# Optimization experiments

Measured on AMD Instinct MI355X. Metric: run time of the kernel, lower is better.

## Reference

```python
import jax, jax.numpy as jnp
import numpy as np

B, N, C, F, E, K = 2, 2048, 1024, 4096, 8, 2

def setup_inputs() -> dict:
    key = jax.random.key(0)
    k = jax.random.split(key, 6)
    xavier1 = float(np.sqrt(6.0 / (C + F)))
    xavier2 = float(np.sqrt(6.0 / (F + C)))
    return {
        "x": jax.random.normal(k[0], (B, N, C), dtype=jnp.float32),
        "router_w": jax.random.normal(k[1], (E, C), dtype=jnp.float32) * 0.01,
        "w1": jax.random.uniform(k[2], (E, F, C), dtype=jnp.float32, minval=-xavier1, maxval=xavier1),
        "b1": jnp.zeros((E, F), dtype=jnp.float32),
        "w2": jax.random.uniform(k[3], (E, C, F), dtype=jnp.float32, minval=-xavier2, maxval=xavier2),
        "b2": jnp.zeros((E, C), dtype=jnp.float32),
    }

def reference(x, router_w, w1, b1, w2, b2):
    Bb, Nn, Cc = x.shape
    x_flat = x.reshape(-1, Cc)                                   # [T, C]
    # Router (eval mode: no noise)
    logits = jnp.einsum('tc,ec->te', x_flat, router_w)           # [T, E]
    probs = jax.nn.softmax(logits, axis=-1)
    top_w, top_idx = jax.lax.top_k(probs, K)                     # [T, K]
    top_w = top_w / (jnp.sum(top_w, axis=-1, keepdims=True) + 1e-9)
    # Dense all-expert MLP (same math as the per-expert gather/scatter loop)
    h = jnp.einsum('tc,efc->tef', x_flat, w1) + b1[None]          # [T, E, F]
    h = jax.nn.relu(h)
    y = jnp.einsum('tef,ecf->tec', h, w2) + b2[None]              # [T, E, C]
    # Gather the K selected experts per token and combine
    sel = jnp.take_along_axis(y, top_idx[:, :, None], axis=1)    # [T, K, C]
    out = jnp.einsum('tkc,tk->tc', sel, top_w)                   # [T, C]
    return out.reshape(Bb, Nn, Cc)
```

## Files before the change

kernel.cpp:

```cpp
#include <hip/hip_runtime.h>
#include <hip/hip_fp16.h>


#define T_TOK 4096
#define C_DIM 1024
#define F_DIM 4096
#define E_NUM 8
#define BM 128
#define BN 256
#define BK 64
#define MAXT 72
#define NP   (MAXT * BM)
#define TILE_H 8192

typedef float f32x4 __attribute__((ext_vector_type(4)));
typedef _Float16 half8 __attribute__((ext_vector_type(8)));

#define AS1 __attribute__((address_space(1)))
#define AS3 __attribute__((address_space(3)))

__device__ __forceinline__ int swz(int r, int ec) { return ec ^ ((r & 7) << 3); }

__device__ __forceinline__ half8 cvt8(float4 f0, float4 f1) {
  half8 hv;
  hv[0] = (_Float16)f0.x; hv[1] = (_Float16)f0.y; hv[2] = (_Float16)f0.z; hv[3] = (_Float16)f0.w;
  hv[4] = (_Float16)f1.x; hv[5] = (_Float16)f1.y; hv[6] = (_Float16)f1.z; hv[7] = (_Float16)f1.w;
  return hv;
}

__device__ __forceinline__ int xcd_swz(int bid, int nwg) {
  int xcd = bid & 7, rest = bid >> 3;
  int q = nwg >> 3, r = nwg & 7;
  return (xcd < r ? xcd * (q + 1) : r * (q + 1) + (xcd - r) * q) + rest;
}

__global__ __launch_bounds__(256) void router_kernel(
    const float* __restrict__ x, const float* __restrict__ rw,
    int* __restrict__ top_idx, float* __restrict__ top_w)
{
  int t = blockIdx.x * 4 + (threadIdx.x >> 6);
  int lane = threadIdx.x & 63;
  const float* xr = x + (size_t)t * C_DIM;
  float acc[E_NUM];
#pragma unroll
  for (int e = 0; e < E_NUM; ++e) acc[e] = 0.f;
  for (int j = 0; j < C_DIM / 64; ++j) {
    int c = j * 64 + lane;
    float xv = xr[c];
#pragma unroll
    for (int e = 0; e < E_NUM; ++e) acc[e] += xv * rw[e * C_DIM + c];
  }
#pragma unroll
  for (int e = 0; e < E_NUM; ++e) {
    float v = acc[e];
#pragma unroll
    for (int off = 32; off > 0; off >>= 1) v += __shfl_xor(v, off);
    acc[e] = v;
  }
  if (lane == 0) {
    float mx = acc[0];
    for (int e = 1; e < E_NUM; ++e) mx = fmaxf(mx, acc[e]);
    float p[E_NUM]; float Z = 0.f;
    for (int e = 0; e < E_NUM; ++e) { p[e] = expf(acc[e] - mx); Z += p[e]; }
    int b0 = 0;
    for (int e = 1; e < E_NUM; ++e) if (p[e] > p[b0]) b0 = e;
    int b1i = -1; float pb = -1.f;
    for (int e = 0; e < E_NUM; ++e) if (e != b0 && p[e] > pb) { pb = p[e]; b1i = e; }
    float p0 = p[b0] / Z, p1 = pb / Z;
    float s = p0 + p1 + 1e-9f;
    top_idx[t * 2 + 0] = b0;
    top_idx[t * 2 + 1] = b1i;
    top_w[t * 2 + 0] = p0 / s;
    top_w[t * 2 + 1] = p1 / s;
  }
}

__global__ void build_lists(const int* __restrict__ top_idx,
                            int* __restrict__ rows_g, int* __restrict__ counts,
                            int* __restrict__ tile_off, int* __restrict__ inv)
{
  int e = threadIdx.x >> 6;
  int lane = threadIdx.x & 63;
  int cnt = 0;
  for (int t0 = 0; t0 < T_TOK; t0 += 64) {
    int t = t0 + lane;
    bool sel = (top_idx[t * 2] == e) || (top_idx[t * 2 + 1] == e);
    cnt += __popcll(__ballot(sel));
  }
  if (lane == 0) counts[e] = cnt;
  __syncthreads();
  if (threadIdx.x == 0) {
    int o = 0;
    for (int i = 0; i < E_NUM; ++i) { tile_off[i] = o; o += (counts[i] + BM - 1) / BM; }
    tile_off[E_NUM] = o;
  }
  __syncthreads();
  int base = tile_off[e] * BM;
  int pos = 0;
  for (int t0 = 0; t0 < T_TOK; t0 += 64) {
    int t = t0 + lane;
    int i0 = top_idx[t * 2], i1 = top_idx[t * 2 + 1];
    bool sel = (i0 == e) || (i1 == e);
    unsigned long long mask = __ballot(sel);
    if (sel) {
      int p = pos + __popcll(mask & ((1ull << lane) - 1ull));
      int slot = t * 2 + ((i0 == e) ? 0 : 1);
      rows_g[base + p] = slot;
      inv[slot] = (e << 16) | (base + p);
    }
    pos += __popcll(mask);
  }
}

__global__ __launch_bounds__(256) void gather_x(
    const float* __restrict__ x, const int* __restrict__ rows_g,
    const int* __restrict__ counts, const int* __restrict__ tile_off,
    _Float16* __restrict__ xg)
{
  unsigned g = blockIdx.x * 256 + threadIdx.x;
  unsigned p = g >> 7, ccr = g & 127;
  int gt = p >> 7, r = p & 127;
  int kc = ccr >> 3, c8 = ccr & 7;
  int e = -1;
#pragma unroll
  for (int i = 0; i < E_NUM; ++i)
    if (gt >= tile_off[i] && gt < tile_off[i + 1]) e = i;
  half8 hv = {};
  if (e >= 0) {
    int nrem = counts[e] - (gt - tile_off[e]) * BM;
    if (r < nrem) {
      int t = rows_g[p] >> 1;
      const float4* s = reinterpret_cast<const float4*>(x + (size_t)t * C_DIM + kc * 64 + c8 * 8);
      hv = cvt8(s[0], s[1]);
    }
  }
  *reinterpret_cast<half8*>(xg + ((size_t)gt * 16 + kc) * TILE_H + r * 64 + ((c8 ^ (r & 7)) << 3)) = hv;
}

__global__ __launch_bounds__(256) void cvt_w1(
    const float* __restrict__ src, _Float16* __restrict__ dst, int ch, int Fc, int lgnftl)
{
  unsigned g = blockIdx.x * 256 + threadIdx.x;
  unsigned tile = g >> 10;
  unsigned kc = tile & 15;
  unsigned et = tile >> 4;
  unsigned ftl = et & ((1u << lgnftl) - 1);
  unsigned e = et >> lgnftl;
  unsigned r = (g >> 3) & 127;
  unsigned sc = g & 7;
  unsigned c8 = sc ^ (r & 7);
  unsigned frow = ftl * 128 + r;
  const float4* s = reinterpret_cast<const float4*>(
      src + ((size_t)e * F_DIM + ch * Fc + frow) * C_DIM + kc * 64 + c8 * 8);
  *reinterpret_cast<half8*>(dst + (size_t)g * 8) = cvt8(s[0], s[1]);
}

__global__ __launch_bounds__(256) void cvt_w2(
    const float* __restrict__ src, _Float16* __restrict__ dst, int ch, int Fc, int lgnkc)
{
  unsigned g = blockIdx.x * 256 + threadIdx.x;
  unsigned tile = g >> 10;
  unsigned kc = tile & ((1u << lgnkc) - 1);
  unsigned et = tile >> lgnkc;
  unsigned ct = et & 7;
  unsigned e = et >> 3;
  unsigned r = (g >> 3) & 127;
  unsigned sc = g & 7;
  unsigned c8 = sc ^ (r & 7);
  unsigned c = ct * 128 + r;
  const float4* s = reinterpret_cast<const float4*>(
      src + ((size_t)e * C_DIM + c) * F_DIM + ch * Fc + kc * 64 + c8 * 8);
  *reinterpret_cast<half8*>(dst + (size_t)g * 8) = cvt8(s[0], s[1]);
}

#define STAGE_TILE(aSrc_, b0Src_, b1Src_)                                         \
  {                                                                               \
    _Pragma("unroll")                                                             \
    for (int i_ = 0; i_ < 2; ++i_) {                                              \
      int o_ = tid * 8 + i_ * 4096;                                               \
      __builtin_amdgcn_global_load_lds((const AS1 void*)((aSrc_) + o_),           \
          (AS3 void*)(&As[o_]), 16, 0, 0);                                        \
      __builtin_amdgcn_global_load_lds((const AS1 void*)((b0Src_) + o_),          \
          (AS3 void*)(&Bs[o_]), 16, 0, 0);                                        \
      __builtin_amdgcn_global_load_lds((const AS1 void*)((b1Src_) + o_),          \
          (AS3 void*)(&Bs[8192 + o_]), 16, 0, 0);                                 \
    }                                                                             \
  }

#define COMPUTE_TILE()                                                            \
  _Pragma("unroll")                                                               \
  for (int kk = 0; kk < BK; kk += 32) {                                           \
    const int klo = kk + (lane >> 4) * 8;                                         \
    half8 aF[4], bF[4];                                                           \
    _Pragma("unroll")                                                             \
    for (int m = 0; m < 4; ++m) {                                                 \
      int r = wr * 64 + m * 16 + (lane & 15);                                     \
      aF[m] = *reinterpret_cast<const half8*>(&As[r * BK + swz(r, klo)]);         \
    }                                                                             \
    _Pragma("unroll")                                                             \
    for (int n = 0; n < 4; ++n) {                                                 \
      int br = wc * 64 + n * 16 + (lane & 15);                                    \
      bF[n] = *reinterpret_cast<const half8*>(                                    \
          &Bs[(br >> 7) * 8192 + (br & 127) * 64 + swz(br, klo)]);                \
    }                                                                             \
    _Pragma("unroll")                                                             \
    for (int m = 0; m < 4; ++m)                                                   \
      _Pragma("unroll")                                                           \
      for (int n = 0; n < 4; ++n)                                                 \
        acc[m][n] = __builtin_amdgcn_mfma_f32_16x16x32_f16(aF[m], bF[n], acc[m][n], 0, 0, 0); \
  }

#define STAGE2(aSrc_, bSrc_)                                                      \
  {                                                                               \
    _Pragma("unroll")                                                             \
    for (int i_ = 0; i_ < 4; ++i_) {                                              \
      int o_ = tid * 8 + i_ * 2048;                                               \
      __builtin_amdgcn_global_load_lds((const AS1 void*)((aSrc_) + o_),           \
          (AS3 void*)(&As[o_]), 16, 0, 0);                                        \
      __builtin_amdgcn_global_load_lds((const AS1 void*)((bSrc_) + o_),           \
          (AS3 void*)(&Bs[o_]), 16, 0, 0);                                        \
    }                                                                             \
  }

#define COMPUTE2()                                                                \
  _Pragma("unroll")                                                               \
  for (int kk = 0; kk < BK; kk += 32) {                                           \
    const int klo = kk + (lane >> 4) * 8;                                         \
    half8 aF[4], bF[4];                                                           \
    _Pragma("unroll")                                                             \
    for (int m = 0; m < 4; ++m) {                                                 \
      int r = wr * 64 + m * 16 + (lane & 15);                                     \
      aF[m] = *reinterpret_cast<const half8*>(&As[r * BK + swz(r, klo)]);         \
    }                                                                             \
    _Pragma("unroll")                                                             \
    for (int n = 0; n < 4; ++n) {                                                 \
      int r = wc * 64 + n * 16 + (lane & 15);                                     \
      bF[n] = *reinterpret_cast<const half8*>(&Bs[r * BK + swz(r, klo)]);         \
    }                                                                             \
    _Pragma("unroll")                                                             \
    for (int m = 0; m < 4; ++m)                                                   \
      _Pragma("unroll")                                                           \
      for (int n = 0; n < 4; ++n)                                                 \
        acc[m][n] = __builtin_amdgcn_mfma_f32_16x16x32_f16(aF[m], bF[n], acc[m][n], 0, 0, 0); \
  }

__global__ __launch_bounds__(512) void gemm1_kernel(
    const _Float16* __restrict__ xg, const _Float16* __restrict__ w1t,
    const float* __restrict__ b1, const int* __restrict__ counts,
    const int* __restrict__ tile_off, _Float16* __restrict__ ht,
    int ch, int Fc)
{
  const int NFT = Fc / BN;
  const int wgid = xcd_swz(blockIdx.x, gridDim.x);
  const int grp = wgid / (8 * NFT);
  const int rem = wgid - grp * 8 * NFT;
  const int ft = rem >> 3;
  const int gt = grp * 8 + (rem & 7);
  if (gt >= tile_off[E_NUM]) return;
  int e = 0;
  while (gt >= tile_off[e + 1]) ++e;
  const int nrem = min(counts[e] - (gt - tile_off[e]) * BM, BM);
  const int nftl = Fc >> 7;
  const _Float16* At  = xg + (size_t)gt * 16 * TILE_H;
  const _Float16* Bt0 = w1t + (size_t)(e * nftl + 2 * ft) * 16 * TILE_H;
  const _Float16* Bt1 = w1t + (size_t)(e * nftl + 2 * ft + 1) * 16 * TILE_H;

  __shared__ __align__(16) _Float16 As[TILE_H];
  __shared__ __align__(16) _Float16 Bs[2 * TILE_H];

  const int tid = threadIdx.x;
  const int lane = tid & 63;
  const int wave = tid >> 6;
  const int wr = wave >> 2, wc = wave & 3;

  f32x4 acc[4][4];
#pragma unroll
  for (int m = 0; m < 4; ++m)
#pragma unroll
    for (int n = 0; n < 4; ++n) acc[m][n] = (f32x4){0.f, 0.f, 0.f, 0.f};

  for (int kc = 0; kc < 16; ++kc) {
    STAGE_TILE(At + (size_t)kc * TILE_H, Bt0 + (size_t)kc * TILE_H, Bt1 + (size_t)kc * TILE_H);
    __syncthreads();
    COMPUTE_TILE();
    __syncthreads();
  }

  const int nkcF = Fc >> 6;
#pragma unroll
  for (int m = 0; m < 4; ++m) {
#pragma unroll
    for (int j = 0; j < 4; ++j) {
      int iloc = wr * 64 + m * 16 + (lane >> 4) * 4 + j;
      if (iloc < nrem) {
#pragma unroll
        for (int n = 0; n < 4; ++n) {
          int fl = ft * BN + wc * 64 + n * 16 + (lane & 15);
          float v = acc[m][n][j] + b1[e * F_DIM + ch * Fc + fl];
          _Float16 h = (_Float16)fmaxf(v, 0.f);
          ht[((size_t)gt * nkcF + (fl >> 6)) * TILE_H + iloc * 64 +
             ((((fl >> 3) & 7) ^ (iloc & 7)) << 3) + (fl & 7)] = h;
        }
      }
    }
  }
}

__global__ __launch_bounds__(256) void gemm2_kernel(
    const _Float16* __restrict__ ht, const _Float16* __restrict__ w2t,
    const int* __restrict__ tile_off, _Float16* __restrict__ y,
    int Fc, int kspl, int accum)
{
  const int NCMB = 8 * kspl;
  const int wgid = xcd_swz(blockIdx.x, gridDim.x);
  const int grp = wgid / (8 * NCMB);
  const int rem = wgid - grp * 8 * NCMB;
  const int cmb = rem >> 3;
  const int gt = grp * 8 + (rem & 7);
  if (gt >= tile_off[E_NUM]) return;
  const int ct = cmb & 7;
  const int ks = cmb >> 3;
  int e = 0;
  while (gt >= tile_off[e + 1]) ++e;
  const int nkc = Fc >> 6;
  const int klen = nkc / kspl;
  const _Float16* At = ht + ((size_t)gt * nkc + ks * klen) * TILE_H;
  const _Float16* Bt = w2t + ((size_t)(e * 8 + ct) * nkc + ks * klen) * TILE_H;

  __shared__ __align__(16) _Float16 As[TILE_H];
  __shared__ __align__(16) _Float16 Bs[TILE_H];

  const int tid = threadIdx.x;
  const int lane = tid & 63;
  const int wave = tid >> 6;
  const int wr = wave >> 1, wc = wave & 1;

  f32x4 acc[4][4];
#pragma unroll
  for (int m = 0; m < 4; ++m)
#pragma unroll
    for (int n = 0; n < 4; ++n) acc[m][n] = (f32x4){0.f, 0.f, 0.f, 0.f};

  for (int kc = 0; kc < klen; ++kc) {
    STAGE2(At + (size_t)kc * TILE_H, Bt + (size_t)kc * TILE_H);
    __syncthreads();
    COMPUTE2();
    __syncthreads();
  }

  _Float16* yk = y + ((size_t)(ks * MAXT + gt) * BM) * C_DIM;
#pragma unroll
  for (int m = 0; m < 4; ++m) {
#pragma unroll
    for (int j = 0; j < 4; ++j) {
      int iloc = wr * 64 + m * 16 + (lane >> 4) * 4 + j;
#pragma unroll
      for (int n = 0; n < 4; ++n) {
        int c = ct * 128 + wc * 64 + n * 16 + (lane & 15);
        _Float16* p = yk + (size_t)iloc * C_DIM + c;
        float v = acc[m][n][j];
        if (accum) v += (float)*p;
        *p = (_Float16)v;
      }
    }
  }
}

__global__ __launch_bounds__(256) void combine_kernel(
    const _Float16* __restrict__ y, const int* __restrict__ inv,
    const float* __restrict__ top_w, const float* __restrict__ b2,
    float* __restrict__ out, int kspl)
{
  int g = blockIdx.x * 256 + threadIdx.x;
  int t = g >> 7, c8 = (g & 127) << 3;
  float o[8];
#pragma unroll
  for (int i = 0; i < 8; ++i) o[i] = 0.f;
#pragma unroll
  for (int k = 0; k < 2; ++k) {
    int iv = inv[t * 2 + k];
    int e = iv >> 16, pos = iv & 0xffff;
    float w = top_w[t * 2 + k];
    const float4* bb = reinterpret_cast<const float4*>(b2 + e * C_DIM + c8);
    float4 bv0 = bb[0], bv1 = bb[1];
    float s[8] = {bv0.x, bv0.y, bv0.z, bv0.w, bv1.x, bv1.y, bv1.z, bv1.w};
    for (int ks = 0; ks < kspl; ++ks) {
      half8 hv = *reinterpret_cast<const half8*>(
          y + ((size_t)(ks * MAXT * BM + pos)) * C_DIM + c8);
#pragma unroll
      for (int i = 0; i < 8; ++i) s[i] += (float)hv[i];
    }
#pragma unroll
    for (int i = 0; i < 8; ++i) o[i] += w * s[i];
  }
  float4* op = reinterpret_cast<float4*>(out + (size_t)t * C_DIM + c8);
  op[0] = (float4){o[0], o[1], o[2], o[3]};
  op[1] = (float4){o[4], o[5], o[6], o[7]};
}

extern "C" void kernel_launch(void* const* d_in, const int* in_sizes, int n_in,
                              void* d_out, int out_size, void* d_ws, size_t ws_size,
                              hipStream_t stream)
{
  const float* x  = (const float*)d_in[0];
  const float* rw = (const float*)d_in[1];
  const float* w1 = (const float*)d_in[2];
  const float* b1 = (const float*)d_in[3];
  const float* w2 = (const float*)d_in[4];
  const float* b2 = (const float*)d_in[5];
  float* out = (float*)d_out;

  char* ws = (char*)d_ws;
  size_t off = 0;
  auto carve = [&](size_t bytes) -> void* {
    void* p = ws + off;
    off += (bytes + 255) & ~(size_t)255;
    return p;
  };
  int*   top_idx  = (int*)carve((size_t)T_TOK * 2 * sizeof(int));
  float* top_w    = (float*)carve((size_t)T_TOK * 2 * sizeof(float));
  int*   counts   = (int*)carve(E_NUM * sizeof(int));
  int*   tile_off = (int*)carve((E_NUM + 1) * sizeof(int));
  int*   rows_g   = (int*)carve((size_t)NP * sizeof(int));
  int*   inv      = (int*)carve((size_t)T_TOK * 2 * sizeof(int));
  _Float16* xg    = (_Float16*)carve((size_t)MAXT * 16 * TILE_H * sizeof(_Float16));
  _Float16* y     = (_Float16*)carve((size_t)2 * NP * C_DIM * sizeof(_Float16));
  size_t fixed = off;

  int nchunk = 8;
  const int cands[4] = {1, 2, 4, 8};
  for (int ci = 0; ci < 4; ++ci) {
    int n = cands[ci];
    size_t fc = (size_t)(F_DIM / n);
    size_t w1b = ((size_t)E_NUM * fc * C_DIM * 2 + 255) & ~(size_t)255;
    size_t w2b = ((size_t)E_NUM * C_DIM * fc * 2 + 255) & ~(size_t)255;
    size_t htb = ((size_t)MAXT * (fc >> 6) * TILE_H * 2 + 255) & ~(size_t)255;
    if (fixed + w1b + w2b + htb <= ws_size) { nchunk = n; break; }
  }
  const int Fc = F_DIM / nchunk;
  int lgFc = 0; while ((1 << lgFc) < Fc) ++lgFc;
  _Float16* w1t = (_Float16*)carve((size_t)E_NUM * Fc * C_DIM * sizeof(_Float16));
  _Float16* w2t = (_Float16*)carve((size_t)E_NUM * C_DIM * Fc * sizeof(_Float16));
  _Float16* ht  = (_Float16*)carve((size_t)MAXT * (Fc >> 6) * TILE_H * sizeof(_Float16));

  const int kspl = (Fc >= 2048) ? 2 : 1;

  router_kernel<<<T_TOK / 4, 256, 0, stream>>>(x, rw, top_idx, top_w);
  build_lists<<<1, 512, 0, stream>>>(top_idx, rows_g, counts, tile_off, inv);
  gather_x<<<(MAXT * BM * 128) / 256, 256, 0, stream>>>(x, rows_g, counts, tile_off, xg);

  const int cvt_blocks = 4 * Fc;
  for (int ch = 0; ch < nchunk; ++ch) {
    cvt_w1<<<cvt_blocks, 256, 0, stream>>>(w1, w1t, ch, Fc, lgFc - 7);
    cvt_w2<<<cvt_blocks, 256, 0, stream>>>(w2, w2t, ch, Fc, lgFc - 6);
    gemm1_kernel<<<MAXT * (Fc / BN), 512, 0, stream>>>(
        xg, w1t, b1, counts, tile_off, ht, ch, Fc);
    gemm2_kernel<<<MAXT * 8 * kspl, 256, 0, stream>>>(
        ht, w2t, tile_off, y, Fc, kspl, ch != 0);
  }
  combine_kernel<<<(T_TOK * 128) / 256, 256, 0, stream>>>(y, inv, top_w, b2, out, kspl);
}
```

Baseline: 355.5 us.

## Swap MFMA operands for vectorized epilogue stores and merge weight conversion kernels

The MFMA operand order is swapped so each lane's four accumulator values lie along the feature/channel dimension. The gemm1 and gemm2 epilogues can then issue half4 stores, float4 bias loads and half4 read-modify-writes instead of scalar per-element accesses. The two weight-conversion kernels are merged into one launch per chunk to cut launch overhead. The gemm1 row-validity check is dropped, so padded rows now write relu(bias) into ht; these rows appear to be discarded downstream.

Result: no change. 352.7 us (-0.8%).

```diff
diff --git a/kernel.cpp b/kernel.cpp
--- a/kernel.cpp
+++ b/kernel.cpp
@@ -15,6 +15,7 @@
 
 typedef float f32x4 __attribute__((ext_vector_type(4)));
 typedef _Float16 half8 __attribute__((ext_vector_type(8)));
+typedef _Float16 half4 __attribute__((ext_vector_type(4)));
 
 #define AS1 __attribute__((address_space(1)))
 #define AS3 __attribute__((address_space(3)))
@@ -137,40 +138,40 @@
   *reinterpret_cast<half8*>(xg + ((size_t)gt * 16 + kc) * TILE_H + r * 64 + ((c8 ^ (r & 7)) << 3)) = hv;
 }
 
-__global__ __launch_bounds__(256) void cvt_w1(
-    const float* __restrict__ src, _Float16* __restrict__ dst, int ch, int Fc, int lgnftl)
+__global__ __launch_bounds__(256) void cvt_w(
+    const float* __restrict__ w1, const float* __restrict__ w2,
+    _Float16* __restrict__ w1t, _Float16* __restrict__ w2t,
+    int ch, int Fc, int lgnftl, int lgnkc, unsigned halfChunks)
 {
   unsigned g = blockIdx.x * 256 + threadIdx.x;
-  unsigned tile = g >> 10;
-  unsigned kc = tile & 15;
-  unsigned et = tile >> 4;
-  unsigned ftl = et & ((1u << lgnftl) - 1);
-  unsigned e = et >> lgnftl;
-  unsigned r = (g >> 3) & 127;
-  unsigned sc = g & 7;
-  unsigned c8 = sc ^ (r & 7);
-  unsigned frow = ftl * 128 + r;
-  const float4* s = reinterpret_cast<const float4*>(
-      src + ((size_t)e * F_DIM + ch * Fc + frow) * C_DIM + kc * 64 + c8 * 8);
-  *reinterpret_cast<half8*>(dst + (size_t)g * 8) = cvt8(s[0], s[1]);
-}
-
-__global__ __launch_bounds__(256) void cvt_w2(
-    const float* __restrict__ src, _Float16* __restrict__ dst, int ch, int Fc, int lgnkc)
-{
-  unsigned g = blockIdx.x * 256 + threadIdx.x;
-  unsigned tile = g >> 10;
-  unsigned kc = tile & ((1u << lgnkc) - 1);
-  unsigned et = tile >> lgnkc;
-  unsigned ct = et & 7;
-  unsigned e = et >> 3;
-  unsigned r = (g >> 3) & 127;
-  unsigned sc = g & 7;
-  unsigned c8 = sc ^ (r & 7);
-  unsigned c = ct * 128 + r;
-  const float4* s = reinterpret_cast<const float4*>(
-      src + ((size_t)e * C_DIM + c) * F_DIM + ch * Fc + kc * 64 + c8 * 8);
-  *reinterpret_cast<half8*>(dst + (size_t)g * 8) = cvt8(s[0], s[1]);
+  if (g < halfChunks) {
+    unsigned tile = g >> 10;
+    unsigned kc = tile & 15;
+    unsigned et = tile >> 4;
+    unsigned ftl = et & ((1u << lgnftl) - 1);
+    unsigned e = et >> lgnftl;
+    unsigned r = (g >> 3) & 127;
+    unsigned sc = g & 7;
+    unsigned c8 = sc ^ (r & 7);
+    unsigned frow = ftl * 128 + r;
+    const float4* s = reinterpret_cast<const float4*>(
+        w1 + ((size_t)e * F_DIM + ch * Fc + frow) * C_DIM + kc * 64 + c8 * 8);
+    *reinterpret_cast<half8*>(w1t + (size_t)g * 8) = cvt8(s[0], s[1]);
+  } else {
+    unsigned g2 = g - halfChunks;
+    unsigned tile = g2 >> 10;
+    unsigned kc = tile & ((1u << lgnkc) - 1);
+    unsigned et = tile >> lgnkc;
+    unsigned ct = et & 7;
+    unsigned e = et >> 3;
+    unsigned r = (g2 >> 3) & 127;
+    unsigned sc = g2 & 7;
+    unsigned c8 = sc ^ (r & 7);
+    unsigned c = ct * 128 + r;
+    const float4* s = reinterpret_cast<const float4*>(
+        w2 + ((size_t)e * C_DIM + c) * F_DIM + ch * Fc + kc * 64 + c8 * 8);
+    *reinterpret_cast<half8*>(w2t + (size_t)g2 * 8) = cvt8(s[0], s[1]);
+  }
 }
 
 #define STAGE_TILE(aSrc_, b0Src_, b1Src_)                                         \
@@ -207,7 +208,7 @@
     for (int m = 0; m < 4; ++m)                                                   \
       _Pragma("unroll")                                                           \
       for (int n = 0; n < 4; ++n)                                                 \
-        acc[m][n] = __builtin_amdgcn_mfma_f32_16x16x32_f16(aF[m], bF[n], acc[m][n], 0, 0, 0); \
+        acc[m][n] = __builtin_amdgcn_mfma_f32_16x16x32_f16(bF[n], aF[m], acc[m][n], 0, 0, 0); \
   }
 
 #define STAGE2(aSrc_, bSrc_)                                                      \
@@ -241,7 +242,7 @@
     for (int m = 0; m < 4; ++m)                                                   \
       _Pragma("unroll")                                                           \
       for (int n = 0; n < 4; ++n)                                                 \
-        acc[m][n] = __builtin_amdgcn_mfma_f32_16x16x32_f16(aF[m], bF[n], acc[m][n], 0, 0, 0); \
+        acc[m][n] = __builtin_amdgcn_mfma_f32_16x16x32_f16(bF[n], aF[m], acc[m][n], 0, 0, 0); \
   }
 
 __global__ __launch_bounds__(512) void gemm1_kernel(
@@ -259,7 +260,6 @@
   if (gt >= tile_off[E_NUM]) return;
   int e = 0;
   while (gt >= tile_off[e + 1]) ++e;
-  const int nrem = min(counts[e] - (gt - tile_off[e]) * BM, BM);
   const int nftl = Fc >> 7;
   const _Float16* At  = xg + (size_t)gt * 16 * TILE_H;
   const _Float16* Bt0 = w1t + (size_t)(e * nftl + 2 * ft) * 16 * TILE_H;
@@ -287,21 +287,22 @@
   }
 
   const int nkcF = Fc >> 6;
+  const float* b1e = b1 + e * F_DIM + ch * Fc;
 #pragma unroll
   for (int m = 0; m < 4; ++m) {
-#pragma unroll
-    for (int j = 0; j < 4; ++j) {
-      int iloc = wr * 64 + m * 16 + (lane >> 4) * 4 + j;
-      if (iloc < nrem) {
-#pragma unroll
-        for (int n = 0; n < 4; ++n) {
-          int fl = ft * BN + wc * 64 + n * 16 + (lane & 15);
-          float v = acc[m][n][j] + b1[e * F_DIM + ch * Fc + fl];
-          _Float16 h = (_Float16)fmaxf(v, 0.f);
-          ht[((size_t)gt * nkcF + (fl >> 6)) * TILE_H + iloc * 64 +
-             ((((fl >> 3) & 7) ^ (iloc & 7)) << 3) + (fl & 7)] = h;
-        }
-      }
+    int tok = wr * 64 + m * 16 + (lane & 15);
+#pragma unroll
+    for (int n = 0; n < 4; ++n) {
+      int flb = ft * BN + wc * 64 + n * 16 + ((lane >> 4) << 2);
+      float4 bv = *reinterpret_cast<const float4*>(b1e + flb);
+      half4 hv;
+      hv[0] = (_Float16)fmaxf(acc[m][n][0] + bv.x, 0.f);
+      hv[1] = (_Float16)fmaxf(acc[m][n][1] + bv.y, 0.f);
+      hv[2] = (_Float16)fmaxf(acc[m][n][2] + bv.z, 0.f);
+      hv[3] = (_Float16)fmaxf(acc[m][n][3] + bv.w, 0.f);
+      *reinterpret_cast<half4*>(
+          ht + ((size_t)gt * nkcF + (flb >> 6)) * TILE_H + tok * 64 +
+          ((((flb >> 3) & 7) ^ (tok & 7)) << 3) + (flb & 7)) = hv;
     }
   }
 }
@@ -351,17 +352,25 @@
   _Float16* yk = y + ((size_t)(ks * MAXT + gt) * BM) * C_DIM;
 #pragma unroll
   for (int m = 0; m < 4; ++m) {
-#pragma unroll
-    for (int j = 0; j < 4; ++j) {
-      int iloc = wr * 64 + m * 16 + (lane >> 4) * 4 + j;
-#pragma unroll
-      for (int n = 0; n < 4; ++n) {
-        int c = ct * 128 + wc * 64 + n * 16 + (lane & 15);
-        _Float16* p = yk + (size_t)iloc * C_DIM + c;
-        float v = acc[m][n][j];
-        if (accum) v += (float)*p;
-        *p = (_Float16)v;
+    int pos = wr * 64 + m * 16 + (lane & 15);
+#pragma unroll
+    for (int n = 0; n < 4; ++n) {
+      int cb = ct * 128 + wc * 64 + n * 16 + ((lane >> 4) << 2);
+      half4* p = reinterpret_cast<half4*>(yk + (size_t)pos * C_DIM + cb);
+      half4 hv;
+      if (accum) {
+        half4 old = *p;
+        hv[0] = (_Float16)(acc[m][n][0] + (float)old[0]);
+        hv[1] = (_Float16)(acc[m][n][1] + (float)old[1]);
+        hv[2] = (_Float16)(acc[m][n][2] + (float)old[2]);
+        hv[3] = (_Float16)(acc[m][n][3] + (float)old[3]);
+      } else {
+        hv[0] = (_Float16)acc[m][n][0];
+        hv[1] = (_Float16)acc[m][n][1];
+        hv[2] = (_Float16)acc[m][n][2];
+        hv[3] = (_Float16)acc[m][n][3];
       }
+      *p = hv;
     }
   }
 }
@@ -449,10 +458,9 @@
   build_lists<<<1, 512, 0, stream>>>(top_idx, rows_g, counts, tile_off, inv);
   gather_x<<<(MAXT * BM * 128) / 256, 256, 0, stream>>>(x, rows_g, counts, tile_off, xg);
 
-  const int cvt_blocks = 4 * Fc;
+  const unsigned halfChunks = (unsigned)Fc << 10;
   for (int ch = 0; ch < nchunk; ++ch) {
-    cvt_w1<<<cvt_blocks, 256, 0, stream>>>(w1, w1t, ch, Fc, lgFc - 7);
-    cvt_w2<<<cvt_blocks, 256, 0, stream>>>(w2, w2t, ch, Fc, lgFc - 6);
+    cvt_w<<<8 * Fc, 256, 0, stream>>>(w1, w2, w1t, w2t, ch, Fc, lgFc - 7, lgFc - 6, halfChunks);
     gemm1_kernel<<<MAXT * (Fc / BN), 512, 0, stream>>>(
         xg, w1t, b1, counts, tile_off, ht, ch, Fc);
     gemm2_kernel<<<MAXT * 8 * kspl, 256, 0, stream>>>(
```
